# Performance work log

Measured on AMD Instinct MI355X. Metric: run time of the kernel, lower is better.

## Reference

```python
import jax, jax.numpy as jnp
import numpy as np

SR = 16000
N_TAPS = 10
MIN_F = 50.0
MAX_F = 2000.0


def setup_inputs() -> dict:
    key = jax.random.key(0)
    k1, k2 = jax.random.split(key)
    x = jax.random.normal(k1, (8, 1, 32000), dtype=jnp.float32)
    # raw f params as in the module: 3*(rand*2-1) in [-3, 3]
    f = 3.0 * (jax.random.uniform(k2, (128, 1), dtype=jnp.float32) * 2.0 - 1.0)
    a = jnp.full((128, 1), 0.9, dtype=jnp.float32)
    return {"x": x, "f": f, "a": a}


def _comb(x, f_raw, a):
    # scaling_function (min_freq/max_freq branch, no bins):
    # f = min_freq * (max_freq/min_freq) ** sigmoid(f_raw)
    fratio = MAX_F / MIN_F
    f = MIN_F * fratio ** jax.nn.sigmoid(f_raw)  # [O, I] fundamental freq in Hz

    B, I, T = x.shape
    O = f.shape[0]
    D = SR / f  # [O, I] fractional delay in samples (one period)
    n = jnp.arange(T, dtype=x.dtype)
    ci = jnp.arange(I)[None, :, None]  # channel index for gather, [1, I, 1]

    acc = jnp.zeros((B, O, T), dtype=x.dtype)
    # y[b,o,t] = sum_i sum_{k=0}^{n_taps-1} a[o,i]^k * lerp(x[b,i, t - k*D[o,i]])
    for k in range(N_TAPS):
        pos = n[None, None, :] - k * D[:, :, None]  # [O, I, T] fractional read positions
        i0 = jnp.floor(pos)
        frac = (pos - i0).astype(x.dtype)
        valid = (i0 >= 0).astype(x.dtype)  # causal: zero before signal start
        i0i = jnp.clip(i0.astype(jnp.int32), 0, T - 1)
        i1i = jnp.clip(i0i + 1, 0, T - 1)
        x0 = x[:, ci, i0i]  # [B, O, I, T]
        x1 = x[:, ci, i1i]  # [B, O, I, T]
        tap = (x0 * (1.0 - frac) + x1 * frac) * valid
        acc = acc + jnp.sum((a ** k)[None, :, :, None] * tap, axis=2)
    return acc


def reference(x, f, a):
    # use_bias=False -> b = 0, gain g unused in forward
    return _comb(x, f, a)
```

## Files before the change

kernel.cpp:

```cpp
#include <hip/hip_runtime.h>
#include <math.h>

#define T_LEN 32000
#define B_N 8
#define O_N 128
#define NTAPS 10
#define TILE_T 1280
#define NT 5
#define PAD 2944
#define NSTAGE (TILE_T + PAD + 1)
#define NSTAGE_AL ((NSTAGE + 3) & ~3)
#define OCHUNK 16

__global__ __launch_bounds__(128) void comb_params_kernel(
    const float* __restrict__ f, const float* __restrict__ a,
    float* __restrict__ tp) {
  int o = threadIdx.x;
  double fr = (double)f[o];
  double sig = 1.0 / (1.0 + exp(-fr));
  float ff = (float)(50.0 * pow(40.0, sig));
  float D = 16000.0f / ff;
  float av = a[o];
  for (int k = 0; k < NTAPS; ++k) {
    tp[o * 20 + k] = (float)k * D;
    tp[o * 20 + 10 + k] = (float)pow((double)av, (double)k);
  }
}

template <bool SAFE>
__device__ __forceinline__ void comb_body(const float* __restrict__ tp,
                                          float* __restrict__ outp,
                                          const float* sx, int oc,
                                          const float* tf, int base_g) {
#pragma unroll 1
  for (int oi = 0; oi < OCHUNK; ++oi) {
    const float* __restrict__ p = tp + (oc + oi) * 20;
    float acc[NT];
#pragma unroll
    for (int j = 0; j < NT; ++j) acc[j] = 0.0f;
    for (int k = 0; k < NTAPS; ++k) {
      float kD = p[k];
      float ak = p[10 + k];
#pragma unroll
      for (int j = 0; j < NT; ++j) {
        float pos = tf[j] - kD;
        float frac = __builtin_amdgcn_fractf(pos);
        int idx = (int)pos - base_g;
        float x0 = sx[idx];
        float x1 = sx[idx + 1];
        float tap = fmaf(frac, x1 - x0, x0);
        if (!SAFE) tap = (pos >= 0.0f) ? tap : 0.0f;
        acc[j] = fmaf(ak, tap, acc[j]);
      }
    }
#pragma unroll
    for (int j = 0; j < NT; ++j)
      outp[(size_t)oi * T_LEN + 256 * j] = acc[j];
  }
}

__global__ __launch_bounds__(256) void comb_main_kernel(
    const float* __restrict__ x, const float* __restrict__ tp,
    float* __restrict__ out) {
  __shared__ float sx[NSTAGE_AL];
  int bx = blockIdx.x;
  int t0 = bx * TILE_T;
  int b = blockIdx.y;
  int oc = blockIdx.z * OCHUNK;
  const float* __restrict__ xrow = x + b * T_LEN;
  int base_g = t0 - PAD;
  int tid = threadIdx.x;

  if (bx >= 3 && bx <= 23) {
    float4* s4 = (float4*)sx;
    const float4* g4 = (const float4*)(xrow + base_g);
#pragma unroll 1
    for (int j = tid; j < NSTAGE_AL / 4; j += 256) s4[j] = g4[j];
  } else {
#pragma unroll 1
    for (int j = tid; j < NSTAGE_AL; j += 256) {
      int g = base_g + j;
      float v = 0.0f;
      if (g >= 0) v = xrow[g < T_LEN - 1 ? g : T_LEN - 1];
      sx[j] = v;
    }
  }
  __syncthreads();

  float tf[NT];
#pragma unroll
  for (int j = 0; j < NT; ++j) tf[j] = (float)(t0 + tid + 256 * j);
  float* outp = out + ((size_t)b * O_N + oc) * T_LEN + t0 + tid;

  if (t0 >= PAD)
    comb_body<true>(tp, outp, sx, oc, tf, base_g);
  else
    comb_body<false>(tp, outp, sx, oc, tf, base_g);
}

extern "C" void kernel_launch(void* const* d_in, const int* in_sizes, int n_in,
                              void* d_out, int out_size, void* d_ws,
                              size_t ws_size, hipStream_t stream) {
  const float* x = (const float*)d_in[0];
  const float* f = (const float*)d_in[1];
  const float* a = (const float*)d_in[2];
  float* out = (float*)d_out;
  float* tp = (float*)d_ws;

  comb_params_kernel<<<1, 128, 0, stream>>>(f, a, tp);

  dim3 grid(T_LEN / TILE_T, B_N, O_N / OCHUNK);
  comb_main_kernel<<<grid, 256, 0, stream>>>(x, tp, out);
}
```

Measured before the change: 197.1 us.

## Hoist per-tap fractional offsets out of time loop and halve output chunk

In the interior fast path, each tap's fractional delay is computed once per block at a reference time instead of once per sample, using the fact that integer time shifts do not change the fractional part. The interpolation weights are folded with the tap gain, and the k=0 tap becomes a direct read. The output-channel chunk is halved to 8, doubling grid size, and the tap parameters are loaded as float4 with the tap loop fully unrolled. This cuts per-sample ALU work but relies on float rounding of pos matching the reference closely enough near integer boundaries.

```diff
diff --git a/kernel.cpp b/kernel.cpp
--- a/kernel.cpp
+++ b/kernel.cpp
@@ -10,7 +10,8 @@
 #define PAD 2944
 #define NSTAGE (TILE_T + PAD + 1)
 #define NSTAGE_AL ((NSTAGE + 3) & ~3)
-#define OCHUNK 16
+#define OCHUNK 8
+#define TC 640
 
 __global__ __launch_bounds__(128) void comb_params_kernel(
     const float* __restrict__ f, const float* __restrict__ a,
@@ -27,30 +28,70 @@
   }
 }
 
-template <bool SAFE>
-__device__ __forceinline__ void comb_body(const float* __restrict__ tp,
-                                          float* __restrict__ outp,
-                                          const float* sx, int oc,
-                                          const float* tf, int base_g) {
+__device__ __forceinline__ void comb_body_fast(const float* __restrict__ tp,
+                                               float* __restrict__ outp,
+                                               const float* sx, int oc,
+                                               int t0, int tid) {
+  float tcf = (float)(t0 + TC);
+  int cbase = PAD - t0 - TC;
+  float xt[NT];
+#pragma unroll
+  for (int j = 0; j < NT; ++j) xt[j] = sx[PAD + tid + 256 * j];
 #pragma unroll 1
   for (int oi = 0; oi < OCHUNK; ++oi) {
-    const float* __restrict__ p = tp + (oc + oi) * 20;
+    const float4* p4 = (const float4*)(tp + (oc + oi) * 20);
+    float4 q0 = p4[0], q1 = p4[1], q2 = p4[2], q3 = p4[3], q4 = p4[4];
+    float kD[NTAPS] = {q0.x, q0.y, q0.z, q0.w, q1.x, q1.y, q1.z, q1.w, q2.x, q2.y};
+    float ak[NTAPS] = {q2.z, q2.w, q3.x, q3.y, q3.z, q3.w, q4.x, q4.y, q4.z, q4.w};
+    float acc[NT];
+#pragma unroll
+    for (int j = 0; j < NT; ++j) acc[j] = xt[j];
+#pragma unroll
+    for (int k = 1; k < NTAPS; ++k) {
+      float pc = tcf - kD[k];
+      float fc = __builtin_amdgcn_fractf(pc);
+      int sb = (int)(pc - fc) + cbase + tid;
+      float w1 = ak[k] * fc;
+      float w0 = ak[k] - w1;
+#pragma unroll
+      for (int j = 0; j < NT; ++j) {
+        int idx = sb + 256 * j;
+        float x0 = sx[idx];
+        float x1 = sx[idx + 1];
+        acc[j] = fmaf(w0, x0, fmaf(w1, x1, acc[j]));
+      }
+    }
+#pragma unroll
+    for (int j = 0; j < NT; ++j)
+      outp[(size_t)oi * T_LEN + 256 * j] = acc[j];
+  }
+}
+
+__device__ __forceinline__ void comb_body_edge(const float* __restrict__ tp,
+                                               float* __restrict__ outp,
+                                               const float* sx, int oc,
+                                               const float* tf, int base_g) {
+#pragma unroll 1
+  for (int oi = 0; oi < OCHUNK; ++oi) {
+    const float4* p4 = (const float4*)(tp + (oc + oi) * 20);
+    float4 q0 = p4[0], q1 = p4[1], q2 = p4[2], q3 = p4[3], q4 = p4[4];
+    float kD[NTAPS] = {q0.x, q0.y, q0.z, q0.w, q1.x, q1.y, q1.z, q1.w, q2.x, q2.y};
+    float ak[NTAPS] = {q2.z, q2.w, q3.x, q3.y, q3.z, q3.w, q4.x, q4.y, q4.z, q4.w};
     float acc[NT];
 #pragma unroll
     for (int j = 0; j < NT; ++j) acc[j] = 0.0f;
+#pragma unroll
     for (int k = 0; k < NTAPS; ++k) {
-      float kD = p[k];
-      float ak = p[10 + k];
 #pragma unroll
       for (int j = 0; j < NT; ++j) {
-        float pos = tf[j] - kD;
+        float pos = tf[j] - kD[k];
         float frac = __builtin_amdgcn_fractf(pos);
         int idx = (int)pos - base_g;
         float x0 = sx[idx];
         float x1 = sx[idx + 1];
         float tap = fmaf(frac, x1 - x0, x0);
-        if (!SAFE) tap = (pos >= 0.0f) ? tap : 0.0f;
-        acc[j] = fmaf(ak, tap, acc[j]);
+        tap = (pos >= 0.0f) ? tap : 0.0f;
+        acc[j] = fmaf(ak[k], tap, acc[j]);
       }
     }
 #pragma unroll
@@ -87,15 +128,16 @@
   }
   __syncthreads();
 
-  float tf[NT];
-#pragma unroll
-  for (int j = 0; j < NT; ++j) tf[j] = (float)(t0 + tid + 256 * j);
   float* outp = out + ((size_t)b * O_N + oc) * T_LEN + t0 + tid;
 
-  if (t0 >= PAD)
-    comb_body<true>(tp, outp, sx, oc, tf, base_g);
-  else
-    comb_body<false>(tp, outp, sx, oc, tf, base_g);
+  if (bx >= 3) {
+    comb_body_fast(tp, outp, sx, oc, t0, tid);
+  } else {
+    float tf[NT];
+#pragma unroll
+    for (int j = 0; j < NT; ++j) tf[j] = (float)(t0 + tid + 256 * j);
+    comb_body_edge(tp, outp, sx, oc, tf, base_g);
+  }
 }
 
 extern "C" void kernel_launch(void* const* d_in, const int* in_sizes, int n_in,
```

Result: faster. 174.0 us (-11.7%).
